# Kernel optimization log

Measured on AMD Instinct MI355X. Metric: run time of the kernel, lower is better.

Reference implementation:

```python
import jax, jax.numpy as jnp
import numpy as np

N = 50000      # nodes
E = 800000     # edges (before self loops)
G = 256        # graphs in batch
N_IN, NHID, HEADS, NOUT = 128, 64, 2, 768
ATT_SLOPE = 0.2   # GATv2 attention LeakyReLU slope (PyG default)
ACT_SLOPE = 0.01  # nn.LeakyReLU default slope


def setup_inputs() -> dict:
    key = jax.random.key(0)
    ks = jax.random.split(key, 20)
    def lin_w(k, fo, fi):
        return (jax.random.normal(k, (fo, fi), jnp.float32) / np.sqrt(fi)).astype(jnp.float32)
    x = jax.random.normal(ks[0], (N, N_IN), jnp.float32)
    edge_index = jax.random.randint(ks[1], (2, E), 0, N, dtype=jnp.int64)
    batch = jnp.sort(jax.random.randint(ks[2], (N,), 0, G, dtype=jnp.int64))
    HC = HEADS * NHID
    return {
        "x": x, "edge_index": edge_index, "batch": batch,
        # conv1: GATv2Conv(N_IN -> NHID, heads=HEADS)
        "w1_l": lin_w(ks[3], HC, N_IN), "b1_l": jnp.zeros((HC,), jnp.float32),
        "w1_r": lin_w(ks[4], HC, N_IN), "b1_r": jnp.zeros((HC,), jnp.float32),
        "att1": jax.random.normal(ks[5], (HEADS, NHID), jnp.float32) / np.sqrt(NHID),
        "bias1": jnp.zeros((HC,), jnp.float32),
        # conv2: GATv2Conv(HC -> NHID, heads=1)
        "w2_l": lin_w(ks[6], NHID, HC), "b2_l": jnp.zeros((NHID,), jnp.float32),
        "w2_r": lin_w(ks[7], NHID, HC), "b2_r": jnp.zeros((NHID,), jnp.float32),
        "att2": jax.random.normal(ks[8], (1, NHID), jnp.float32) / np.sqrt(NHID),
        "bias2": jnp.zeros((NHID,), jnp.float32),
        # MLP head
        "fc1_w": lin_w(ks[9], NHID, NHID), "fc1_b": jnp.zeros((NHID,), jnp.float32),
        "fc2_w": lin_w(ks[10], NOUT, NHID), "fc2_b": jnp.zeros((NOUT,), jnp.float32),
    }


def _leaky(v, slope):
    return jnp.where(v > 0, v, slope * v)


def gatv2_conv(x, src, dst, w_l, b_l, w_r, b_r, att, bias, heads, ch):
    n = x.shape[0]
    xl = (x @ w_l.T + b_l).reshape(n, heads, ch)   # source transform
    xr = (x @ w_r.T + b_r).reshape(n, heads, ch)   # target transform
    m = _leaky(xl[src] + xr[dst], ATT_SLOPE)       # [E, H, C]
    e = jnp.einsum('ehc,hc->eh', m, att)           # attention logits
    # segment softmax over incoming edges of each dst node (self loops guarantee non-empty)
    emax = jax.ops.segment_max(e, dst, num_segments=n)
    ex = jnp.exp(e - emax[dst])
    denom = jax.ops.segment_sum(ex, dst, num_segments=n)
    alpha = ex / denom[dst]
    out = jax.ops.segment_sum(xl[src] * alpha[:, :, None], dst, num_segments=n)
    return out.reshape(n, heads * ch) + bias


def reference(x, edge_index, batch, w1_l, b1_l, w1_r, b1_r, att1, bias1,
              w2_l, b2_l, w2_r, b2_r, att2, bias2, fc1_w, fc1_b, fc2_w, fc2_b):
    loops = jnp.arange(N, dtype=edge_index.dtype)
    src = jnp.concatenate([edge_index[0], loops])  # PyG adds self loops by default
    dst = jnp.concatenate([edge_index[1], loops])
    h = gatv2_conv(x, src, dst, w1_l, b1_l, w1_r, b1_r, att1, bias1, HEADS, NHID)
    h = _leaky(h, ACT_SLOPE)
    h = gatv2_conv(h, src, dst, w2_l, b2_l, w2_r, b2_r, att2, bias2, 1, NHID)
    h = _leaky(h, ACT_SLOPE)
    # global mean pool over graphs
    sums = jax.ops.segment_sum(h, batch, num_segments=G)
    cnt = jax.ops.segment_sum(jnp.ones((N,), h.dtype), batch, num_segments=G)
    pooled = sums / jnp.maximum(cnt, 1.0)[:, None]
    h = _leaky(pooled @ fc1_w.T + fc1_b, ACT_SLOPE)
    return h @ fc2_w.T + fc2_b
```

## Files before the change

kernel.cpp:

```cpp
#include <hip/hip_runtime.h>

#define ATT_SLOPE 0.2f
#define ACT_SLOPE 0.01f

typedef _Float16 half8  __attribute__((ext_vector_type(8)));
typedef _Float16 half2v __attribute__((ext_vector_type(2)));
typedef float    floatx4 __attribute__((ext_vector_type(4)));

#if defined(__has_builtin)
#if __has_builtin(__builtin_amdgcn_fdot2)
#define HAVE_FDOT2 1
#endif
#endif

__device__ __forceinline__ float lrelu(float v, float s) {
    return fmaxf(v, v * s);
}

__device__ __forceinline__ half2v lrelu2(half2v m) {
    half2v t = m * (_Float16)ATT_SLOPE;
    return __builtin_elementwise_max(m, t);
}

__device__ __forceinline__ float dot2(half2v a, half2v b, float c) {
#ifdef HAVE_FDOT2
    return __builtin_amdgcn_fdot2(a, b, c, false);
#else
    return c + (float)a[0] * (float)b[0] + (float)a[1] * (float)b[1];
#endif
}


__global__ __launch_bounds__(256) void k_count_rank(const int* __restrict__ ei, int E, int N,
                                                    int* __restrict__ deg,
                                                    int* __restrict__ rank) {
    int i = blockIdx.x * 256 + threadIdx.x;
    int total = E + N;
    if (i >= total) return;
    int dst = (i < E) ? ei[E + i] : (i - E);
    rank[i] = atomicAdd(&deg[dst], 1);
}

__global__ __launch_bounds__(256) void k_scan_block(const int* __restrict__ deg, int n,
                                                    int* __restrict__ rp1, int* __restrict__ bsum) {
    __shared__ int s[256];
    int tid = threadIdx.x;
    int i = blockIdx.x * 256 + tid;
    s[tid] = (i < n) ? deg[i] : 0;
    __syncthreads();
    for (int off = 1; off < 256; off <<= 1) {
        int t = (tid >= off) ? s[tid - off] : 0;
        __syncthreads();
        s[tid] += t;
        __syncthreads();
    }
    if (i < n) rp1[i] = s[tid];
    if (tid == 255) bsum[blockIdx.x] = s[255];
}

__global__ __launch_bounds__(256) void k_scan_add(int* __restrict__ rowptr,
                                                  const int* __restrict__ bsum, int n) {
    __shared__ int s[256];
    int tid = threadIdx.x, bid = blockIdx.x;
    s[tid] = (tid < bid) ? bsum[tid] : 0;
    __syncthreads();
    for (int off = 128; off > 0; off >>= 1) {
        if (tid < off) s[tid] += s[tid + off];
        __syncthreads();
    }
    int boff = s[0];
    int i = bid * 256 + tid;
    if (i < n) rowptr[i + 1] += boff;
    if (i == 0) rowptr[0] = 0;
}


__global__ __launch_bounds__(256) void k_encode_w(const float* __restrict__ w1l,
                                                  const float* __restrict__ w1r,
                                                  const float* __restrict__ w2l,
                                                  const float* __restrict__ w2r,
                                                  _Float16* __restrict__ W1h,
                                                  _Float16* __restrict__ W1lo,
                                                  _Float16* __restrict__ W2h,
                                                  _Float16* __restrict__ W2lo,
                                                  float* __restrict__ gsum, int gn,
                                                  int* __restrict__ deg, int n) {
    int i = blockIdx.x * 256 + threadIdx.x;
    if (i >= 49152 + gn + n) return;
    if (i >= 49152 + gn) {
        deg[i - 49152 - gn] = 0;
        return;
    }
    if (i >= 49152) {
        gsum[i - 49152] = 0.f;
        return;
    }
    float v;
    _Float16 *ph, *pl;
    int idx;
    if (i < 32768) {
        idx = i;
        v = (i < 16384) ? w1l[i] : w1r[i - 16384];
        ph = W1h; pl = W1lo;
    } else {
        int j = i - 32768;
        idx = j;
        v = (j < 8192) ? w2l[j] : w2r[j - 8192];
        ph = W2h; pl = W2lo;
    }
    _Float16 h = (_Float16)v;
    ph[idx] = h;
    pl[idx] = (_Float16)(v - (float)h);
}


template <int COUT, bool IN_F32>
__device__ __forceinline__ void gemm_body(int bid, int tid,
                                          _Float16 (*sWh)[40], _Float16 (*sWl)[40],
                                          const float* __restrict__ Af,
                                          const _Float16* __restrict__ Ahi,
                                          const _Float16* __restrict__ Alo, int n_rows,
                                          const _Float16* __restrict__ Whi,
                                          const _Float16* __restrict__ Wlo,
                                          const float* __restrict__ B0,
                                          const float* __restrict__ B1,
                                          _Float16* __restrict__ out) {
    constexpr int NT = COUT / 16;
    const int lane = tid & 63, wv = tid >> 6;
    const int m = lane & 15, q = lane >> 4;
    const long row0 = ((long)bid * 4 + wv) * 16;
    const bool active = row0 < n_rows;
    const long arow = row0 + m;

    floatx4 acc[NT] = {};
    for (int kk = 0; kk < 128; kk += 32) {
        __syncthreads();
        for (int t = tid; t < COUT * 4; t += 256) {
            int c = t >> 2, ch = t & 3;
            *(half8*)&sWh[c][ch * 8] = *(const half8*)&Whi[(size_t)c * 128 + kk + ch * 8];
            *(half8*)&sWl[c][ch * 8] = *(const half8*)&Wlo[(size_t)c * 128 + kk + ch * 8];
        }
        __syncthreads();
        if (active) {
            half8 ah, al;
            if constexpr (IN_F32) {
                float4 a0 = *(const float4*)&Af[(size_t)arow * 128 + kk + q * 8];
                float4 a1 = *(const float4*)&Af[(size_t)arow * 128 + kk + q * 8 + 4];
                float av[8] = {a0.x, a0.y, a0.z, a0.w, a1.x, a1.y, a1.z, a1.w};
                #pragma unroll
                for (int x = 0; x < 8; ++x) {
                    ah[x] = (_Float16)av[x];
                    al[x] = (_Float16)(av[x] - (float)ah[x]);
                }
            } else {
                ah = *(const half8*)&Ahi[(size_t)arow * 128 + kk + q * 8];
                al = *(const half8*)&Alo[(size_t)arow * 128 + kk + q * 8];
            }
            #pragma unroll
            for (int nt = 0; nt < NT; ++nt) {
                half8 bh = *(const half8*)&sWh[nt * 16 + m][q * 8];
                half8 bl = *(const half8*)&sWl[nt * 16 + m][q * 8];
                acc[nt] = __builtin_amdgcn_mfma_f32_16x16x32_f16(ah, bh, acc[nt], 0, 0, 0);
                acc[nt] = __builtin_amdgcn_mfma_f32_16x16x32_f16(al, bh, acc[nt], 0, 0, 0);
                acc[nt] = __builtin_amdgcn_mfma_f32_16x16x32_f16(ah, bl, acc[nt], 0, 0, 0);
            }
        }
    }
    if (active) {
        #pragma unroll
        for (int nt = 0; nt < NT; ++nt) {
            int col = nt * 16 + m;
            float b = (col < COUT / 2) ? B0[col] : B1[col - COUT / 2];
            #pragma unroll
            for (int r = 0; r < 4; ++r) {
                long grow = row0 + q * 4 + r;
                out[(size_t)grow * COUT + col] = (_Float16)(acc[nt][r] + b);
            }
        }
    }
}

__global__ __launch_bounds__(256) void k_gemm1_scatter(const float* __restrict__ x,
                                                       const _Float16* __restrict__ W1h,
                                                       const _Float16* __restrict__ W1lo,
                                                       const float* __restrict__ B0,
                                                       const float* __restrict__ B1,
                                                       _Float16* __restrict__ buf1, int n_rows,
                                                       const int* __restrict__ ei, int E,
                                                       const int* __restrict__ rowptr,
                                                       const int* __restrict__ rank,
                                                       int* __restrict__ adj, int gB) {
    __shared__ _Float16 sWh[256][40];
    __shared__ _Float16 sWl[256][40];
    const int bid = blockIdx.x, tid = threadIdx.x;
    if (bid < gB) {
        gemm_body<256, true>(bid, tid, sWh, sWl, x, nullptr, nullptr, n_rows,
                             W1h, W1lo, B0, B1, buf1);
    } else {
        int i = (bid - gB) * 256 + tid;
        int T = E + n_rows;
        if (i < T) {
            int dst = (i < E) ? ei[E + i] : (i - E);
            int src = (i < E) ? ei[i] : dst;
            adj[rowptr[dst] + rank[i]] = src;
        }
    }
}

template <int COUT, bool IN_F32>
__global__ __launch_bounds__(256) void gemm_mfma(const float* __restrict__ Af,
                                                 const _Float16* __restrict__ Ahi,
                                                 const _Float16* __restrict__ Alo, int n_rows,
                                                 const _Float16* __restrict__ Whi,
                                                 const _Float16* __restrict__ Wlo,
                                                 const float* __restrict__ B0,
                                                 const float* __restrict__ B1,
                                                 _Float16* __restrict__ out) {
    __shared__ _Float16 sWh[COUT][40];
    __shared__ _Float16 sWl[COUT][40];
    gemm_body<COUT, IN_F32>(blockIdx.x, threadIdx.x, sWh, sWl, Af, Ahi, Alo, n_rows,
                            Whi, Wlo, B0, B1, out);
}


__global__ __launch_bounds__(128) void conv1_fused(const _Float16* __restrict__ buf,
                                                   const int* __restrict__ rowptr,
                                                   const int* __restrict__ adj,
                                                   const float* __restrict__ att,
                                                   const float* __restrict__ bias,
                                                   _Float16* __restrict__ h1hi,
                                                   _Float16* __restrict__ h1lo, int n) {
    __shared__ _Float16 sxl[2][16][136];
    __shared__ _Float16 sxr[2][128];
    __shared__ float    sw[2][2][16];
    __shared__ _Float16 satt[128];
    const int tid = threadIdx.x, lane = tid & 63, wv = tid >> 6;
    satt[tid] = (_Float16)att[tid];
    __syncthreads();
    int node = blockIdx.x * 2 + wv;
    if (node >= n) return;

    const int jlane = lane & 15;
    const int grp = lane >> 4;
    const int chq = grp * 32;
    const int head = grp >> 1;
    const int wselg = lane >> 5;
    if (lane < 16)
        *(half8*)&sxr[wv][lane * 8] = *(const half8*)&buf[(size_t)node * 256 + 128 + lane * 8];
    asm volatile("s_waitcnt lgkmcnt(0)" ::: "memory");

    const int s = rowptr[node], e = rowptr[node + 1];
    float2 accA = {0.f, 0.f}, accB = {0.f, 0.f};
    float denA = 0.f, denB = 0.f;
    for (int c0 = s; c0 < e; c0 += 16) {
        const int cnt = min(16, e - c0);
        float sacc0 = 0.f, sacc1 = 0.f;
        if (jlane < cnt) {
            int src = adj[c0 + jlane];
            const _Float16* xlp = &buf[(size_t)src * 256 + chq];
            #pragma unroll
            for (int k = 0; k < 4; ++k) {
                half8 l = *(const half8*)&xlp[k * 8];
                half8 r = *(const half8*)&sxr[wv][chq + k * 8];
                half8 a = *(const half8*)&satt[chq + k * 8];
                *(half8*)&sxl[wv][jlane][chq + k * 8] = l;
                float* sp = (k & 1) ? &sacc1 : &sacc0;
                #pragma unroll
                for (int p = 0; p < 4; ++p) {
                    half2v lp = {l[2 * p], l[2 * p + 1]};
                    half2v rp = {r[2 * p], r[2 * p + 1]};
                    half2v ap = {a[2 * p], a[2 * p + 1]};
                    *sp = dot2(lrelu2(lp + rp), ap, *sp);
                }
            }
        }
        float sacc = sacc0 + sacc1;
        float efull = sacc + __shfl_xor(sacc, 16);
        if ((grp & 1) == 0 && jlane < cnt) sw[wv][head][jlane] = __expf(efull);
        asm volatile("s_waitcnt lgkmcnt(0)" ::: "memory");
        int j = 0;
        for (; j + 1 < cnt; j += 2) {
            float w0 = sw[wv][wselg][j], w1 = sw[wv][wselg][j + 1];
            half2v v0 = *(const half2v*)&sxl[wv][j][lane * 2];
            half2v v1 = *(const half2v*)&sxl[wv][j + 1][lane * 2];
            accA.x += w0 * (float)v0[0]; accA.y += w0 * (float)v0[1]; denA += w0;
            accB.x += w1 * (float)v1[0]; accB.y += w1 * (float)v1[1]; denB += w1;
        }
        if (j < cnt) {
            float w0 = sw[wv][wselg][j];
            half2v v0 = *(const half2v*)&sxl[wv][j][lane * 2];
            accA.x += w0 * (float)v0[0]; accA.y += w0 * (float)v0[1]; denA += w0;
        }
        asm volatile("s_waitcnt lgkmcnt(0)" ::: "memory");
    }
    float inv = 1.f / (denA + denB);
    float2 b = *(const float2*)&bias[lane * 2];
    float ox = lrelu((accA.x + accB.x) * inv + b.x, ACT_SLOPE);
    float oy = lrelu((accA.y + accB.y) * inv + b.y, ACT_SLOPE);
    half2v hv, lv;
    hv[0] = (_Float16)ox; lv[0] = (_Float16)(ox - (float)hv[0]);
    hv[1] = (_Float16)oy; lv[1] = (_Float16)(oy - (float)hv[1]);
    *(half2v*)&h1hi[(size_t)node * 128 + lane * 2] = hv;
    *(half2v*)&h1lo[(size_t)node * 128 + lane * 2] = lv;
}


__global__ __launch_bounds__(128) void conv2_fused(const _Float16* __restrict__ buf,
                                                   const int* __restrict__ rowptr,
                                                   const int* __restrict__ adj,
                                                   const float* __restrict__ att,
                                                   const float* __restrict__ bias,
                                                   const int* __restrict__ batch,
                                                   float* __restrict__ gsum, int n) {
    __shared__ _Float16 sxl[2][16][72];
    __shared__ _Float16 sxr[2][64];
    __shared__ float    sw[2][16];
    __shared__ _Float16 satt[64];
    const int tid = threadIdx.x, lane = tid & 63, wv = tid >> 6;
    if (tid < 64) satt[tid] = (_Float16)att[tid];
    __syncthreads();
    int node = blockIdx.x * 2 + wv;
    if (node >= n) return;

    const int jlane = lane & 15;
    const int grp = lane >> 4;
    const int chq = grp * 16;
    if (lane < 8)
        *(half8*)&sxr[wv][lane * 8] = *(const half8*)&buf[(size_t)node * 128 + 64 + lane * 8];
    asm volatile("s_waitcnt lgkmcnt(0)" ::: "memory");

    const int s = rowptr[node], e = rowptr[node + 1];
    float accA = 0.f, accB = 0.f, denA = 0.f, denB = 0.f;
    for (int c0 = s; c0 < e; c0 += 16) {
        const int cnt = min(16, e - c0);
        float sacc = 0.f;
        if (jlane < cnt) {
            int src = adj[c0 + jlane];
            const _Float16* xlp = &buf[(size_t)src * 128 + chq];
            #pragma unroll
            for (int k = 0; k < 2; ++k) {
                half8 l = *(const half8*)&xlp[k * 8];
                half8 r = *(const half8*)&sxr[wv][chq + k * 8];
                half8 a = *(const half8*)&satt[chq + k * 8];
                *(half8*)&sxl[wv][jlane][chq + k * 8] = l;
                #pragma unroll
                for (int p = 0; p < 4; ++p) {
                    half2v lp = {l[2 * p], l[2 * p + 1]};
                    half2v rp = {r[2 * p], r[2 * p + 1]};
                    half2v ap = {a[2 * p], a[2 * p + 1]};
                    sacc = dot2(lrelu2(lp + rp), ap, sacc);
                }
            }
        }
        float s1 = sacc + __shfl_xor(sacc, 16);
        float efull = s1 + __shfl_xor(s1, 32);
        if (grp == 0 && jlane < cnt) sw[wv][jlane] = __expf(efull);
        asm volatile("s_waitcnt lgkmcnt(0)" ::: "memory");
        int j = 0;
        for (; j + 1 < cnt; j += 2) {
            float w0 = sw[wv][j], w1 = sw[wv][j + 1];
            accA += w0 * (float)sxl[wv][j][lane];     denA += w0;
            accB += w1 * (float)sxl[wv][j + 1][lane]; denB += w1;
        }
        if (j < cnt) {
            float w0 = sw[wv][j];
            accA += w0 * (float)sxl[wv][j][lane];
            denA += w0;
        }
        asm volatile("s_waitcnt lgkmcnt(0)" ::: "memory");
    }
    float val = lrelu((accA + accB) / (denA + denB) + bias[lane], ACT_SLOPE);
    atomicAdd(&gsum[(size_t)batch[node] * 64 + lane], val);
}


__device__ __forceinline__ int lower_bound(const int* a, int n, int v) {
    int lo = 0, hi = n;
    while (lo < hi) { int mid = (lo + hi) >> 1; if (a[mid] < v) lo = mid + 1; else hi = mid; }
    return lo;
}

__global__ __launch_bounds__(256) void pool_mlp(const float* __restrict__ gsum,
                                                const int* __restrict__ batch,
                                                const float* __restrict__ fc1_w,
                                                const float* __restrict__ fc1_b,
                                                const float* __restrict__ fc2_w,
                                                const float* __restrict__ fc2_b,
                                                float* __restrict__ out, int n) {
    const int g = blockIdx.x;
    const int tid = threadIdx.x;
    __shared__ float pooled[64];
    __shared__ float hmid[64];

    int lo = lower_bound(batch, n, g);
    int hi = lower_bound(batch, n, g + 1);
    float inv = 1.f / (float)max(hi - lo, 1);

    if (tid < 64) pooled[tid] = gsum[(size_t)g * 64 + tid] * inv;
    __syncthreads();
    if (tid < 64) {
        float acc = fc1_b[tid];
        const float* w = &fc1_w[(size_t)tid * 64];
        #pragma unroll
        for (int k = 0; k < 64; ++k) acc += pooled[k] * w[k];
        hmid[tid] = lrelu(acc, ACT_SLOPE);
    }
    __syncthreads();
    for (int o = tid; o < 768; o += 256) {
        float acc = fc2_b[o];
        const float* w = &fc2_w[(size_t)o * 64];
        #pragma unroll
        for (int k = 0; k < 64; ++k) acc += hmid[k] * w[k];
        out[(size_t)g * 768 + o] = acc;
    }
}


extern "C" void kernel_launch(void* const* d_in, const int* in_sizes, int n_in,
                              void* d_out, int out_size, void* d_ws, size_t ws_size,
                              hipStream_t stream) {
    const float* x     = (const float*)d_in[0];
    const int*   ei    = (const int*)d_in[1];
    const int*   batch = (const int*)d_in[2];
    const float* w1_l  = (const float*)d_in[3];
    const float* b1_l  = (const float*)d_in[4];
    const float* w1_r  = (const float*)d_in[5];
    const float* b1_r  = (const float*)d_in[6];
    const float* att1  = (const float*)d_in[7];
    const float* bias1 = (const float*)d_in[8];
    const float* w2_l  = (const float*)d_in[9];
    const float* b2_l  = (const float*)d_in[10];
    const float* w2_r  = (const float*)d_in[11];
    const float* b2_r  = (const float*)d_in[12];
    const float* att2  = (const float*)d_in[13];
    const float* bias2 = (const float*)d_in[14];
    const float* fc1_w = (const float*)d_in[15];
    const float* fc1_b = (const float*)d_in[16];
    const float* fc2_w = (const float*)d_in[17];
    const float* fc2_b = (const float*)d_in[18];
    float* out = (float*)d_out;

    const int N = in_sizes[2];
    const int E = in_sizes[1] / 2;
    const int T = E + N;
    const int G = out_size / 768;

    char* ws = (char*)d_ws;
    size_t off = 0;
    auto alloc = [&](size_t bytes) -> void* {
        void* p = ws + off;
        off = (off + bytes + 255) & ~(size_t)255;
        return p;
    };
    int*      deg    = (int*)alloc((size_t)N * 4);
    int*      rowptr = (int*)alloc((size_t)(N + 1) * 4);
    int*      rank   = (int*)alloc((size_t)T * 4);
    int*      bsum   = (int*)alloc(1024);
    int*      adj    = (int*)alloc((size_t)T * 4);
    _Float16* h1hi   = (_Float16*)alloc((size_t)N * 128 * 2);
    _Float16* h1lo   = (_Float16*)alloc((size_t)N * 128 * 2);
    _Float16* W1h    = (_Float16*)alloc(32768 * 2);
    _Float16* W1lo   = (_Float16*)alloc(32768 * 2);
    _Float16* W2h    = (_Float16*)alloc(16384 * 2);
    _Float16* W2lo   = (_Float16*)alloc(16384 * 2);
    float*    gsum   = (float*)alloc((size_t)G * 64 * 4);
    _Float16* buf1   = (_Float16*)alloc((size_t)N * 256 * 2);
    _Float16* buf2 = buf1;

    const int nbN  = (N + 255) / 256;
    const int nbT  = (T + 255) / 256;
    const int mfmG = (N / 16 + 3) / 4;
    const int edgG = (N + 1) / 2;
    const int encG = (49152 + G * 64 + N + 255) / 256;

    k_encode_w<<<encG, 256, 0, stream>>>(w1_l, w1_r, w2_l, w2_r,
                                         W1h, W1lo, W2h, W2lo, gsum, G * 64, deg, N);

    k_count_rank<<<nbT, 256, 0, stream>>>(ei, E, N, deg, rank);
    k_scan_block<<<nbN, 256, 0, stream>>>(deg, N, rowptr + 1, bsum);
    k_scan_add<<<nbN, 256, 0, stream>>>(rowptr, bsum, N);

    k_gemm1_scatter<<<mfmG + nbT, 256, 0, stream>>>(x, W1h, W1lo, b1_l, b1_r, buf1, N,
                                                    ei, E, rowptr, rank, adj, mfmG);

    conv1_fused<<<edgG, 128, 0, stream>>>(buf1, rowptr, adj, att1, bias1, h1hi, h1lo, N);

    gemm_mfma<128, false><<<mfmG, 256, 0, stream>>>(nullptr, h1hi, h1lo, N,
                                                    W2h, W2lo, b2_l, b2_r, buf2);
    conv2_fused<<<edgG, 128, 0, stream>>>(buf2, rowptr, adj, att2, bias2, batch, gsum, N);

    pool_mlp<<<G, 256, 0, stream>>>(gsum, batch, fc1_w, fc1_b, fc2_w, fc2_b, out, N);
}
```

Baseline: 294.0 us.

## Overlap degree counting with gemm1 and widen conv2 edge chunk to 32

The atomic degree count and rank pass now runs inside the gemm1 launch alongside the MFMA blocks, and the adjacency scatter moves to its own kernel after the scan. The aim is to hide the atomic-heavy counting behind the dense GEMM instead of the scatter. Separately, conv2 handles 32 neighbours per chunk with each lane covering 32 channels, which cuts loop iterations and one shuffle but doubles shared memory per block. The launch count stays the same, and the scatter pass is no longer overlapped with the GEMM.

```diff
diff --git a/kernel.cpp b/kernel.cpp
--- a/kernel.cpp
+++ b/kernel.cpp
@@ -31,16 +31,6 @@
 }
 
 
-__global__ __launch_bounds__(256) void k_count_rank(const int* __restrict__ ei, int E, int N,
-                                                    int* __restrict__ deg,
-                                                    int* __restrict__ rank) {
-    int i = blockIdx.x * 256 + threadIdx.x;
-    int total = E + N;
-    if (i >= total) return;
-    int dst = (i < E) ? ei[E + i] : (i - E);
-    rank[i] = atomicAdd(&deg[dst], 1);
-}
-
 __global__ __launch_bounds__(256) void k_scan_block(const int* __restrict__ deg, int n,
                                                     int* __restrict__ rp1, int* __restrict__ bsum) {
     __shared__ int s[256];
@@ -72,6 +62,18 @@
     int i = bid * 256 + tid;
     if (i < n) rowptr[i + 1] += boff;
     if (i == 0) rowptr[0] = 0;
+}
+
+__global__ __launch_bounds__(256) void k_scatter(const int* __restrict__ ei, int E, int N,
+                                                 const int* __restrict__ rowptr,
+                                                 const int* __restrict__ rank,
+                                                 int* __restrict__ adj) {
+    int i = blockIdx.x * 256 + threadIdx.x;
+    int T = E + N;
+    if (i >= T) return;
+    int dst = (i < E) ? ei[E + i] : (i - E);
+    int src = (i < E) ? ei[i] : dst;
+    adj[rowptr[dst] + rank[i]] = src;
 }
 
 
@@ -180,16 +182,15 @@
     }
 }
 
-__global__ __launch_bounds__(256) void k_gemm1_scatter(const float* __restrict__ x,
-                                                       const _Float16* __restrict__ W1h,
-                                                       const _Float16* __restrict__ W1lo,
-                                                       const float* __restrict__ B0,
-                                                       const float* __restrict__ B1,
-                                                       _Float16* __restrict__ buf1, int n_rows,
-                                                       const int* __restrict__ ei, int E,
-                                                       const int* __restrict__ rowptr,
-                                                       const int* __restrict__ rank,
-                                                       int* __restrict__ adj, int gB) {
+__global__ __launch_bounds__(256) void k_gemm1_cr(const float* __restrict__ x,
+                                                  const _Float16* __restrict__ W1h,
+                                                  const _Float16* __restrict__ W1lo,
+                                                  const float* __restrict__ B0,
+                                                  const float* __restrict__ B1,
+                                                  _Float16* __restrict__ buf1, int n_rows,
+                                                  const int* __restrict__ ei, int E,
+                                                  int* __restrict__ deg,
+                                                  int* __restrict__ rank, int gB) {
     __shared__ _Float16 sWh[256][40];
     __shared__ _Float16 sWl[256][40];
     const int bid = blockIdx.x, tid = threadIdx.x;
@@ -198,11 +199,10 @@
                              W1h, W1lo, B0, B1, buf1);
     } else {
         int i = (bid - gB) * 256 + tid;
-        int T = E + n_rows;
-        if (i < T) {
+        int total = E + n_rows;
+        if (i < total) {
             int dst = (i < E) ? ei[E + i] : (i - E);
-            int src = (i < E) ? ei[i] : dst;
-            adj[rowptr[dst] + rank[i]] = src;
+            rank[i] = atomicAdd(&deg[dst], 1);
         }
     }
 }
@@ -312,9 +312,9 @@
                                                    const float* __restrict__ bias,
                                                    const int* __restrict__ batch,
                                                    float* __restrict__ gsum, int n) {
-    __shared__ _Float16 sxl[2][16][72];
+    __shared__ _Float16 sxl[2][32][72];
     __shared__ _Float16 sxr[2][64];
-    __shared__ float    sw[2][16];
+    __shared__ float    sw[2][32];
     __shared__ _Float16 satt[64];
     const int tid = threadIdx.x, lane = tid & 63, wv = tid >> 6;
     if (tid < 64) satt[tid] = (_Float16)att[tid];
@@ -322,27 +322,27 @@
     int node = blockIdx.x * 2 + wv;
     if (node >= n) return;
 
-    const int jlane = lane & 15;
-    const int grp = lane >> 4;
-    const int chq = grp * 16;
+    const int j = lane & 31;
+    const int g = lane >> 5;
+    const int ch0 = g * 32;
     if (lane < 8)
         *(half8*)&sxr[wv][lane * 8] = *(const half8*)&buf[(size_t)node * 128 + 64 + lane * 8];
     asm volatile("s_waitcnt lgkmcnt(0)" ::: "memory");
 
     const int s = rowptr[node], e = rowptr[node + 1];
     float accA = 0.f, accB = 0.f, denA = 0.f, denB = 0.f;
-    for (int c0 = s; c0 < e; c0 += 16) {
-        const int cnt = min(16, e - c0);
+    for (int c0 = s; c0 < e; c0 += 32) {
+        const int cnt = min(32, e - c0);
         float sacc = 0.f;
-        if (jlane < cnt) {
-            int src = adj[c0 + jlane];
-            const _Float16* xlp = &buf[(size_t)src * 128 + chq];
+        if (j < cnt) {
+            int src = adj[c0 + j];
+            const _Float16* xlp = &buf[(size_t)src * 128 + ch0];
             #pragma unroll
-            for (int k = 0; k < 2; ++k) {
+            for (int k = 0; k < 4; ++k) {
                 half8 l = *(const half8*)&xlp[k * 8];
-                half8 r = *(const half8*)&sxr[wv][chq + k * 8];
-                half8 a = *(const half8*)&satt[chq + k * 8];
-                *(half8*)&sxl[wv][jlane][chq + k * 8] = l;
+                half8 r = *(const half8*)&sxr[wv][ch0 + k * 8];
+                half8 a = *(const half8*)&satt[ch0 + k * 8];
+                *(half8*)&sxl[wv][j][ch0 + k * 8] = l;
                 #pragma unroll
                 for (int p = 0; p < 4; ++p) {
                     half2v lp = {l[2 * p], l[2 * p + 1]};
@@ -352,19 +352,18 @@
                 }
             }
         }
-        float s1 = sacc + __shfl_xor(sacc, 16);
-        float efull = s1 + __shfl_xor(s1, 32);
-        if (grp == 0 && jlane < cnt) sw[wv][jlane] = __expf(efull);
+        float efull = sacc + __shfl_xor(sacc, 32);
+        if (g == 0 && j < cnt) sw[wv][j] = __expf(efull);
         asm volatile("s_waitcnt lgkmcnt(0)" ::: "memory");
-        int j = 0;
-        for (; j + 1 < cnt; j += 2) {
-            float w0 = sw[wv][j], w1 = sw[wv][j + 1];
-            accA += w0 * (float)sxl[wv][j][lane];     denA += w0;
-            accB += w1 * (float)sxl[wv][j + 1][lane]; denB += w1;
-        }
-        if (j < cnt) {
-            float w0 = sw[wv][j];
-            accA += w0 * (float)sxl[wv][j][lane];
+        int jj = 0;
+        for (; jj + 1 < cnt; jj += 2) {
+            float w0 = sw[wv][jj], w1 = sw[wv][jj + 1];
+            accA += w0 * (float)sxl[wv][jj][lane];     denA += w0;
+            accB += w1 * (float)sxl[wv][jj + 1][lane]; denB += w1;
+        }
+        if (jj < cnt) {
+            float w0 = sw[wv][jj];
+            accA += w0 * (float)sxl[wv][jj][lane];
             denA += w0;
         }
         asm volatile("s_waitcnt lgkmcnt(0)" ::: "memory");
@@ -476,12 +475,12 @@
     k_encode_w<<<encG, 256, 0, stream>>>(w1_l, w1_r, w2_l, w2_r,
                                          W1h, W1lo, W2h, W2lo, gsum, G * 64, deg, N);
 
-    k_count_rank<<<nbT, 256, 0, stream>>>(ei, E, N, deg, rank);
+    k_gemm1_cr<<<mfmG + nbT, 256, 0, stream>>>(x, W1h, W1lo, b1_l, b1_r, buf1, N,
+                                               ei, E, deg, rank, mfmG);
+
     k_scan_block<<<nbN, 256, 0, stream>>>(deg, N, rowptr + 1, bsum);
     k_scan_add<<<nbN, 256, 0, stream>>>(rowptr, bsum, N);
-
-    k_gemm1_scatter<<<mfmG + nbT, 256, 0, stream>>>(x, W1h, W1lo, b1_l, b1_r, buf1, N,
-                                                    ei, E, rowptr, rank, adj, mfmG);
+    k_scatter<<<nbT, 256, 0, stream>>>(ei, E, N, rowptr, rank, adj);
 
     conv1_fused<<<edgG, 128, 0, stream>>>(buf1, rowptr, adj, att1, bias1, h1hi, h1lo, N);
 
```

New measurement: 293.9 us. About the same (-0.0%).
